# Kernel tuning notes

Hardware: AMD Instinct MI355X
Metric: run time of the kernel (lower is better)

The kernel has to match this reference:

```python
import jax, jax.numpy as jnp
import numpy as np

EOS_IDX = 2
B, LAYERS, HEADS, SEQ = 1, 33, 20, 512


def setup_inputs() -> dict:
    key = jax.random.key(0)
    k1, k2, k3, k4 = jax.random.split(key, 4)
    tokens = jax.random.randint(k1, (B, SEQ), 0, 30)
    attentions = jax.random.normal(k2, (B, LAYERS, HEADS, SEQ, SEQ), dtype=jnp.float32)
    weight = jax.random.normal(k3, (LAYERS * HEADS,), dtype=jnp.float32) * 0.05
    bias = jax.random.normal(k4, (1,), dtype=jnp.float32) * 0.05
    return {"tokens": tokens, "attentions": attentions, "weight": weight, "bias": bias}


def reference(tokens, attentions, weight, bias):
    b, nl, nh, s, _ = attentions.shape
    # mask out positions at/after EOS token pairs
    eos = (tokens != EOS_IDX).astype(attentions.dtype)           # [B, S]
    mask2d = eos[:, None, :] * eos[:, :, None]                   # [B, S, S]
    att = attentions * mask2d[:, None, None, :, :]
    # [..., :-1, :-1] then [..., 1:, 1:] == drop first and last positions
    att = att[..., 1:-1, 1:-1]                                   # [B, L, H, S-2, S-2]
    att = att.reshape(b, nl * nh, s - 2, s - 2)                  # [B, F, s2, s2]
    # symmetrize
    sym = att + jnp.swapaxes(att, -1, -2)
    # average product correction
    a1 = sym.sum(-1, keepdims=True)                              # [B, F, s2, 1]
    a2 = sym.sum(-2, keepdims=True)                              # [B, F, 1, s2]
    a12 = sym.sum((-1, -2), keepdims=True)                       # [B, F, 1, 1]
    norm = sym - a1 * a2 / a12
    logits = jnp.einsum('bfij,f->bij', norm, weight) + bias[0]
    return jax.nn.sigmoid(logits)                                # [B, s2, s2]
```

## Files before the change

### kernel.cpp

```cpp
#include <hip/hip_runtime.h>
#include <math.h>

#define SEQ   512
#define NF    660
#define CROP  510
#define EOSI  2
#define RT    16
#define GH    20
#define NT_   32
#define NG    33

typedef float f4 __attribute__((ext_vector_type(4)));

#define LOADB(d0, d1, ptr) do {                                               \
    d0 = *(const f4*)(ptr);                                                   \
    d1 = *(const f4*)((ptr) + 64);                                            \
} while (0)

#define CONS(x0, x1, b, h) do {                                               \
    float vals[8] = {x0[0], x0[1], x0[2], x0[3],                              \
                     x1[0], x1[1], x1[2], x1[3]};                             \
    float rs = 0.f;                                                           \
    const float mb = mrow[b];                                                 \
    _Pragma("unroll")                                                         \
    for (int e = 0; e < 8; ++e) {                                             \
        const float v = vals[e];                                              \
        wa_acc[b][e] += wf * v;                                               \
        rs += mskv[e] * v;                                                    \
        cacc[e] += mb * v;                                                    \
    }                                                                         \
    rs += __shfl_xor(rs, 1, 64);                                              \
    rs += __shfl_xor(rs, 2, 64);                                              \
    rs += __shfl_xor(rs, 4, 64);                                              \
    rs += __shfl_xor(rs, 8, 64);                                              \
    if (c8 == 0) rowpart[h][(b) * 4 + r][wave] = rs;                          \
} while (0)

__global__ __launch_bounds__(256) void pass1_kernel(
    const float* __restrict__ A, const int* __restrict__ tokens,
    const float* __restrict__ weight,
    float* __restrict__ WApart, float* __restrict__ rowsum, float* __restrict__ colpart)
{
    __shared__ float msk[SEQ];
    __shared__ float colstage[GH][SEQ];
    __shared__ float rowpart[GH][RT][4];

    const int t = blockIdx.x, g = blockIdx.y;
    const int tid = threadIdx.x, wave = tid >> 6, lane = tid & 63;
    const int r = lane >> 4, c8 = lane & 15;
    const int fbase = g * GH;
    const int row0 = t * RT;
    const int col0 = wave * 128;

    for (int j = tid; j < SEQ; j += 256)
        msk[j] = (j >= 1 && j <= SEQ - 2 && tokens[j] != EOSI) ? 1.f : 0.f;
    __syncthreads();

    float mskv[8];
    #pragma unroll
    for (int p = 0; p < 2; ++p)
        #pragma unroll
        for (int k = 0; k < 4; ++k)
            mskv[p * 4 + k] = msk[col0 + p * 64 + c8 * 4 + k];
    float mrow[4];
    #pragma unroll
    for (int b = 0; b < 4; ++b) mrow[b] = msk[row0 + b * 4 + r];

    float wa_acc[4][8];
    #pragma unroll
    for (int b = 0; b < 4; ++b)
        #pragma unroll
        for (int e = 0; e < 8; ++e) wa_acc[b][e] = 0.f;

    const size_t lofs = (size_t)(row0 + r) * SEQ + col0 + c8 * 4;

    f4 a0, a1, b0, b1;
    {
        const float* Ah = A + ((size_t)fbase << 18) + lofs;
        LOADB(a0, a1, Ah);
    }

    #pragma unroll 1
    for (int h = 0; h < GH; ++h) {
        const float wf = weight[fbase + h];
        const float* __restrict__ Ah = A + ((size_t)(fbase + h) << 18) + lofs;
        float cacc[8] = {0, 0, 0, 0, 0, 0, 0, 0};

        LOADB(b0, b1, Ah + 2048);
        CONS(a0, a1, 0, h);
        LOADB(a0, a1, Ah + 4096);
        CONS(b0, b1, 1, h);
        LOADB(b0, b1, Ah + 6144);
        CONS(a0, a1, 2, h);
        if (h < GH - 1) LOADB(a0, a1, Ah + 262144);
        CONS(b0, b1, 3, h);

        #pragma unroll
        for (int e = 0; e < 8; ++e) {
            cacc[e] += __shfl_xor(cacc[e], 16, 64);
            cacc[e] += __shfl_xor(cacc[e], 32, 64);
        }
        if (r == 0) {
            f4 s = {cacc[0], cacc[1], cacc[2], cacc[3]};
            *(f4*)&colstage[h][col0 + c8 * 4] = s;
        } else if (r == 1) {
            f4 s = {cacc[4], cacc[5], cacc[6], cacc[7]};
            *(f4*)&colstage[h][col0 + 64 + c8 * 4] = s;
        }
    }

    __syncthreads();

    {
        float* __restrict__ dst = colpart + ((size_t)t * NF + fbase) * SEQ;
        const float* __restrict__ src = &colstage[0][0];
        #pragma unroll
        for (int it = 0; it < 10; ++it) {
            const int fl = (it * 256 + tid) * 4;
            *(f4*)(dst + fl) = *(const f4*)(src + fl);
        }
    }
    #pragma unroll
    for (int it = 0; it < 2; ++it) {
        const int e = it * 256 + tid;
        if (e < GH * RT) {
            const int h = e >> 4, i = e & 15;
            rowsum[((size_t)(fbase + h) << 9) + row0 + i] =
                rowpart[h][i][0] + rowpart[h][i][1] + rowpart[h][i][2] + rowpart[h][i][3];
        }
    }
    {
        float* __restrict__ wp = WApart + (size_t)g * SEQ * SEQ + lofs;
        #pragma unroll
        for (int b = 0; b < 4; ++b) {
            f4 o0 = {wa_acc[b][0], wa_acc[b][1], wa_acc[b][2], wa_acc[b][3]};
            f4 o1 = {wa_acc[b][4], wa_acc[b][5], wa_acc[b][6], wa_acc[b][7]};
            float* dst = wp + (size_t)b * 4 * SEQ;
            *(f4*)dst = o0;
            *(f4*)(dst + 64) = o1;
        }
    }
}

__global__ __launch_bounds__(512) void kernel2(
    const float* __restrict__ WApart, float* __restrict__ WA,
    const float* __restrict__ rowsum, const float* __restrict__ colpart,
    const int* __restrict__ tokens, const float* __restrict__ weight,
    float* __restrict__ a1, float* __restrict__ sfac)
{
    __shared__ float part[8];
    const int b = blockIdx.x, tid = threadIdx.x;
    if (b < 128) {
        const size_t idx4 = (size_t)b * 512 + tid;
        f4 a = *(const f4*)(WApart + 4 * idx4);
        #pragma unroll 8
        for (int g = 1; g < NG; ++g) {
            f4 x = *(const f4*)(WApart + (size_t)g * (SEQ * SEQ) + 4 * idx4);
            a += x;
        }
        *(f4*)(WA + 4 * idx4) = a;
    } else {
        const int f = b - 128, j = tid;
        float cs = 0.f;
        #pragma unroll 8
        for (int t = 0; t < NT_; ++t)
            cs += colpart[((size_t)t * NF + f) * SEQ + j];
        const float m = (j >= 1 && j <= SEQ - 2 && tokens[j] != EOSI) ? 1.f : 0.f;
        const float v = m * (rowsum[((size_t)f << 9) + j] + cs);
        a1[((size_t)f << 9) + j] = v;
        float s = v;
        #pragma unroll
        for (int off = 32; off > 0; off >>= 1)
            s += __shfl_down(s, off, 64);
        const int wave = tid >> 6, lane = tid & 63;
        if (lane == 0) part[wave] = s;
        __syncthreads();
        if (tid == 0) {
            float a12 = 0.f;
            #pragma unroll
            for (int k = 0; k < 8; ++k) a12 += part[k];
            sfac[f] = weight[f] / a12;
        }
    }
}

__global__ __launch_bounds__(256) void pass3_kernel(
    const float* __restrict__ WA, const float* __restrict__ a1,
    const float* __restrict__ sfac, const int* __restrict__ tokens,
    const float* __restrict__ bias, float* __restrict__ out)
{
    const int TI = blockIdx.y * 16;
    const int TJ = blockIdx.x * 16;
    const int tid = threadIdx.x;
    const int tx = tid & 15, ty = tid >> 4;

    __shared__ float u_s[32][17];
    __shared__ float v_s[32][17];

    float acc = 0.f;

    for (int f0 = 0; f0 < NF; f0 += 32) {
        #pragma unroll
        for (int c = 0; c < 4; ++c) {
            const int e = c * 256 + tid;
            const int arr = e >> 9, ff = (e >> 4) & 31, ii = e & 15;
            const int f = f0 + ff;
            float val = 0.f;
            if (f < NF) {
                if (arr == 0) {
                    int Iu = TI + 1 + ii; if (Iu > SEQ - 1) Iu = SEQ - 1;
                    val = a1[((size_t)f << 9) + Iu] * sfac[f];
                } else {
                    int Ju = TJ + 1 + ii; if (Ju > SEQ - 1) Ju = SEQ - 1;
                    val = a1[((size_t)f << 9) + Ju];
                }
            }
            if (arr == 0) u_s[ff][ii] = val; else v_s[ff][ii] = val;
        }
        __syncthreads();
        #pragma unroll
        for (int ff = 0; ff < 32; ++ff)
            acc += u_s[ff][ty] * v_s[ff][tx];
        __syncthreads();
    }

    const int i = TI + ty, j = TJ + tx;
    if (i < CROP && j < CROP) {
        const int I = i + 1, J = j + 1;
        const float mi = (tokens[I] != EOSI) ? 1.f : 0.f;
        const float mj = (tokens[J] != EOSI) ? 1.f : 0.f;
        const float first = mi * mj * (WA[((size_t)I << 9) + J] + WA[((size_t)J << 9) + I]);
        const float logit = first - acc + bias[0];
        out[(size_t)i * CROP + j] = 1.f / (1.f + expf(-logit));
    }
}

extern "C" void kernel_launch(void* const* d_in, const int* in_sizes, int n_in,
                              void* d_out, int out_size, void* d_ws, size_t ws_size,
                              hipStream_t stream) {
    const int*   tokens = (const int*)d_in[0];
    const float* A      = (const float*)d_in[1];
    const float* weight = (const float*)d_in[2];
    const float* bias   = (const float*)d_in[3];
    float* out = (float*)d_out;

    float* WApart  = (float*)d_ws;
    float* colpart = WApart + (size_t)NG * SEQ * SEQ;
    float* WA      = colpart + (size_t)NT_ * NF * SEQ;
    float* rowsum  = WA + (size_t)SEQ * SEQ;
    float* a1      = rowsum + (size_t)NF * SEQ;
    float* sfac    = a1 + (size_t)NF * SEQ;

    dim3 g1(NT_, NG);
    pass1_kernel<<<g1, 256, 0, stream>>>(A, tokens, weight, WApart, rowsum, colpart);

    kernel2<<<128 + NF, 512, 0, stream>>>(WApart, WA, rowsum, colpart, tokens, weight, a1, sfac);

    dim3 g3(32, 32);
    pass3_kernel<<<g3, 256, 0, stream>>>(WA, a1, sfac, tokens, bias, out);
}
```

Baseline: 214.9 us.

## Double row tile per block and store per-group weighted partials in fp16

Row tile grows from 16 to 32 rows per block, halving the number of row tiles. This halves the column-partial buffer written by pass1 and summed in kernel2. The per-group weighted-sum partials are now stored as half precision and widened back to float in the reduction kernel, halving that intermediate traffic. The cost is more registers per thread (wa_acc doubles), which may lower occupancy, fewer blocks in pass1 (16x33), and precision loss from fp16 partials.

Result: slower. 246.9 us (+14.9%).

```diff
diff --git a/kernel.cpp b/kernel.cpp
--- a/kernel.cpp
+++ b/kernel.cpp
@@ -5,12 +5,13 @@
 #define NF    660
 #define CROP  510
 #define EOSI  2
-#define RT    16
+#define RT    32
 #define GH    20
-#define NT_   32
+#define NT_   16
 #define NG    33
 
-typedef float f4 __attribute__((ext_vector_type(4)));
+typedef float    f4 __attribute__((ext_vector_type(4)));
+typedef _Float16 h4 __attribute__((ext_vector_type(4)));
 
 #define LOADB(d0, d1, ptr) do {                                               \
     d0 = *(const f4*)(ptr);                                                   \
@@ -39,7 +40,8 @@
 __global__ __launch_bounds__(256) void pass1_kernel(
     const float* __restrict__ A, const int* __restrict__ tokens,
     const float* __restrict__ weight,
-    float* __restrict__ WApart, float* __restrict__ rowsum, float* __restrict__ colpart)
+    _Float16* __restrict__ WApart, float* __restrict__ rowsum,
+    float* __restrict__ colpart)
 {
     __shared__ float msk[SEQ];
     __shared__ float colstage[GH][SEQ];
@@ -62,13 +64,13 @@
         #pragma unroll
         for (int k = 0; k < 4; ++k)
             mskv[p * 4 + k] = msk[col0 + p * 64 + c8 * 4 + k];
-    float mrow[4];
-    #pragma unroll
-    for (int b = 0; b < 4; ++b) mrow[b] = msk[row0 + b * 4 + r];
-
-    float wa_acc[4][8];
-    #pragma unroll
-    for (int b = 0; b < 4; ++b)
+    float mrow[8];
+    #pragma unroll
+    for (int b = 0; b < 8; ++b) mrow[b] = msk[row0 + b * 4 + r];
+
+    float wa_acc[8][8];
+    #pragma unroll
+    for (int b = 0; b < 8; ++b)
         #pragma unroll
         for (int e = 0; e < 8; ++e) wa_acc[b][e] = 0.f;
 
@@ -86,14 +88,15 @@
         const float* __restrict__ Ah = A + ((size_t)(fbase + h) << 18) + lofs;
         float cacc[8] = {0, 0, 0, 0, 0, 0, 0, 0};
 
-        LOADB(b0, b1, Ah + 2048);
-        CONS(a0, a1, 0, h);
-        LOADB(a0, a1, Ah + 4096);
-        CONS(b0, b1, 1, h);
-        LOADB(b0, b1, Ah + 6144);
-        CONS(a0, a1, 2, h);
+        LOADB(b0, b1, Ah + 2048);              CONS(a0, a1, 0, h);
+        LOADB(a0, a1, Ah + 4096);              CONS(b0, b1, 1, h);
+        LOADB(b0, b1, Ah + 6144);              CONS(a0, a1, 2, h);
+        LOADB(a0, a1, Ah + 8192);              CONS(b0, b1, 3, h);
+        LOADB(b0, b1, Ah + 10240);             CONS(a0, a1, 4, h);
+        LOADB(a0, a1, Ah + 12288);             CONS(b0, b1, 5, h);
+        LOADB(b0, b1, Ah + 14336);             CONS(a0, a1, 6, h);
         if (h < GH - 1) LOADB(a0, a1, Ah + 262144);
-        CONS(b0, b1, 3, h);
+        CONS(b0, b1, 7, h);
 
         #pragma unroll
         for (int e = 0; e < 8; ++e) {
@@ -121,29 +124,31 @@
         }
     }
     #pragma unroll
-    for (int it = 0; it < 2; ++it) {
+    for (int it = 0; it < 3; ++it) {
         const int e = it * 256 + tid;
         if (e < GH * RT) {
-            const int h = e >> 4, i = e & 15;
+            const int h = e >> 5, i = e & 31;
             rowsum[((size_t)(fbase + h) << 9) + row0 + i] =
                 rowpart[h][i][0] + rowpart[h][i][1] + rowpart[h][i][2] + rowpart[h][i][3];
         }
     }
     {
-        float* __restrict__ wp = WApart + (size_t)g * SEQ * SEQ + lofs;
-        #pragma unroll
-        for (int b = 0; b < 4; ++b) {
-            f4 o0 = {wa_acc[b][0], wa_acc[b][1], wa_acc[b][2], wa_acc[b][3]};
-            f4 o1 = {wa_acc[b][4], wa_acc[b][5], wa_acc[b][6], wa_acc[b][7]};
-            float* dst = wp + (size_t)b * 4 * SEQ;
-            *(f4*)dst = o0;
-            *(f4*)(dst + 64) = o1;
+        _Float16* __restrict__ wp = WApart + (size_t)g * SEQ * SEQ + lofs;
+        #pragma unroll
+        for (int b = 0; b < 8; ++b) {
+            h4 o0 = {(_Float16)wa_acc[b][0], (_Float16)wa_acc[b][1],
+                     (_Float16)wa_acc[b][2], (_Float16)wa_acc[b][3]};
+            h4 o1 = {(_Float16)wa_acc[b][4], (_Float16)wa_acc[b][5],
+                     (_Float16)wa_acc[b][6], (_Float16)wa_acc[b][7]};
+            _Float16* dst = wp + (size_t)b * 4 * SEQ;
+            *(h4*)dst = o0;
+            *(h4*)(dst + 64) = o1;
         }
     }
 }
 
 __global__ __launch_bounds__(512) void kernel2(
-    const float* __restrict__ WApart, float* __restrict__ WA,
+    const _Float16* __restrict__ WApart, float* __restrict__ WA,
     const float* __restrict__ rowsum, const float* __restrict__ colpart,
     const int* __restrict__ tokens, const float* __restrict__ weight,
     float* __restrict__ a1, float* __restrict__ sfac)
@@ -152,11 +157,14 @@
     const int b = blockIdx.x, tid = threadIdx.x;
     if (b < 128) {
         const size_t idx4 = (size_t)b * 512 + tid;
-        f4 a = *(const f4*)(WApart + 4 * idx4);
+        const h4* __restrict__ src = (const h4*)WApart;
+        h4 x = src[idx4];
+        f4 a = {(float)x[0], (float)x[1], (float)x[2], (float)x[3]};
         #pragma unroll 8
         for (int g = 1; g < NG; ++g) {
-            f4 x = *(const f4*)(WApart + (size_t)g * (SEQ * SEQ) + 4 * idx4);
-            a += x;
+            h4 y = src[(size_t)g * (SEQ * SEQ / 4) + idx4];
+            a[0] += (float)y[0]; a[1] += (float)y[1];
+            a[2] += (float)y[2]; a[3] += (float)y[3];
         }
         *(f4*)(WA + 4 * idx4) = a;
     } else {
@@ -244,8 +252,8 @@
     const float* bias   = (const float*)d_in[3];
     float* out = (float*)d_out;
 
-    float* WApart  = (float*)d_ws;
-    float* colpart = WApart + (size_t)NG * SEQ * SEQ;
+    _Float16* WApart  = (_Float16*)d_ws;
+    float* colpart = (float*)(WApart + (size_t)NG * SEQ * SEQ);
     float* WA      = colpart + (size_t)NT_ * NF * SEQ;
     float* rowsum  = WA + (size_t)SEQ * SEQ;
     float* a1      = rowsum + (size_t)NF * SEQ;
```
